# Kernel tuning notes

Measured on AMD Instinct MI355X. Metric: run time of the kernel, lower is better.

Reference implementation:

```python
import jax, jax.numpy as jnp
from jax import lax
import numpy as np

B, T, H = 128, 512, 512  # batch, seq_length, hidden_dim (== input_dim)


def _xavier(key, shape):
    fan_in, fan_out = shape[1], shape[0]
    limit = float(np.sqrt(6.0 / (fan_in + fan_out)))
    return jax.random.uniform(key, shape, jnp.float32, -limit, limit)


def setup_inputs() -> dict:
    key = jax.random.key(0)
    ks = jax.random.split(key, 10)
    s = 1.0 / np.sqrt(H)  # torch LSTM default init range
    return {
        "x": jax.random.normal(ks[0], (B, T, H), jnp.float32),
        "W_ih": jax.random.uniform(ks[1], (4 * H, H), jnp.float32, -s, s),
        "W_hh": jax.random.uniform(ks[2], (4 * H, H), jnp.float32, -s, s),
        "b_ih": jax.random.uniform(ks[3], (4 * H,), jnp.float32, -s, s),
        "b_hh": jax.random.uniform(ks[4], (4 * H,), jnp.float32, -s, s),
        "Ve": _xavier(ks[5], (1, H)),
        "U1": _xavier(ks[6], (H, 2 * H)),
        "U2": _xavier(ks[7], (H, H)),
        "W_out": _xavier(ks[8], (2, H)),
        "b_out": jnp.zeros((2,), jnp.float32),
    }


def _lstm(x, W_ih, W_hh, b_ih, b_hh):
    # x: [B, T, D] -> hidden states [B, T, H]; PyTorch gate order i,f,g,o
    b = b_ih + b_hh
    # precompute input projections for all timesteps: [T, B, 4H]
    xg = jnp.einsum('btd,gd->tbg', x, W_ih) + b

    def step(carry, xt):
        h, c = carry
        g = xt + h @ W_hh.T  # [B, 4H]
        i, f, gg, o = jnp.split(g, 4, axis=1)
        c = jax.nn.sigmoid(f) * c + jax.nn.sigmoid(i) * jnp.tanh(gg)
        h = jax.nn.sigmoid(o) * jnp.tanh(c)
        return (h, c), h

    h0 = jnp.zeros((x.shape[0], W_hh.shape[1]), x.dtype)
    (_, _), hs = lax.scan(step, (h0, h0), xg)
    return jnp.swapaxes(hs, 0, 1)  # [B, T, H]


def reference(x, W_ih, W_hh, b_ih, b_hh, Ve, U1, U2, W_out, b_out):
    h = _lstm(x, W_ih, W_hh, b_ih, b_hh)  # [B, T, H]
    h_last = h[:, -1, :]  # [B, H]
    # additive attention, vectorized over all timesteps
    Hdim = h.shape[-1]
    u1 = jnp.einsum('bth,gh->btg', h, U1[:, :Hdim]) + jnp.einsum('bh,gh->bg', h_last, U1[:, Hdim:])[:, None, :]
    u2 = jnp.einsum('btd,gd->btg', x, U2)
    u = jnp.tanh(u1 + u2)  # [B, T, H]
    e = jnp.einsum('bth,h->bt', u, Ve[0])
    alpha = jax.nn.softmax(e, axis=1)  # [B, T]
    context = jnp.einsum('bt,bth->bh', alpha, h)  # [B, H]
    params = context @ W_out.T + b_out  # [B, 2]
    mu = params[:, 0]
    sigma = jax.nn.softplus(params[:, 1]) + 1e-5
    return (mu, sigma)
```

## Files before the change

### kernel.cpp

```cpp
#include <hip/hip_runtime.h>
#include <stdint.h>


using short8  = __attribute__((ext_vector_type(8))) short;
using short4v = __attribute__((ext_vector_type(4))) short;
using floatx4 = __attribute__((ext_vector_type(4))) float;

#define MFMA16(a, b, c) __builtin_amdgcn_mfma_f32_16x16x32_bf16((a), (b), (c), 0, 0, 0)

__device__ __forceinline__ unsigned short f2b(float f) {
    unsigned u = __float_as_uint(f);
    u += 0x7FFFu + ((u >> 16) & 1u);
    return (unsigned short)(u >> 16);
}
__device__ __forceinline__ float b2f(unsigned short h) {
    return __uint_as_float(((unsigned)h) << 16);
}
__device__ __forceinline__ float sigm(float x) { return 1.0f / (1.0f + __expf(-x)); }
__device__ __forceinline__ float tanh_(float x) { return 1.0f - 2.0f / (__expf(2.0f * x) + 1.0f); }

__global__ __launch_bounds__(256) void prep_w(
    const float* __restrict__ Wih, const float* __restrict__ bih,
    const float* __restrict__ bhh,
    unsigned short* __restrict__ Wih_bf, float* __restrict__ bias)
{
    const int total = 1048576 + 2048;
    for (int i = blockIdx.x * 256 + threadIdx.x; i < total;
         i += gridDim.x * 256) {
        if (i < 1048576) Wih_bf[i] = f2b(Wih[i]);
        else             bias[i - 1048576] = bih[i - 1048576] + bhh[i - 1048576];
    }
}

__device__ __forceinline__ void gemm_core(
    const unsigned short* __restrict__ A, long long lda,
    const unsigned short* __restrict__ Bm, long long ldb,
    unsigned short* __restrict__ C, long long ldc,
    const float* __restrict__ bias, int mode,
    int m0, int n0, int tid, unsigned short* sbuf)
{
    unsigned short* At = sbuf;
    unsigned short* Bt = sbuf + 128 * 72;
    unsigned short* Ct = sbuf;

    const int wv = tid >> 6, lane = tid & 63, l15 = lane & 15, q = lane >> 4;
    const int wm = wv & 1, wn = wv >> 1;

    floatx4 acc[4][4];
    for (int i = 0; i < 4; i++)
        for (int j = 0; j < 4; j++) acc[i][j] = (floatx4){0.f, 0.f, 0.f, 0.f};

    for (int k0 = 0; k0 < 512; k0 += 64) {
        for (int p = 0; p < 4; p++) {
            int idx = tid + p * 256;
            int row = idx >> 3, ch = idx & 7;
            *(short8*)&At[row * 72 + ch * 8] =
                *(const short8*)&A[(long long)(m0 + row) * lda + k0 + ch * 8];
            *(short8*)&Bt[row * 72 + ch * 8] =
                *(const short8*)&Bm[(long long)(n0 + row) * ldb + k0 + ch * 8];
        }
        __syncthreads();
        for (int ks = 0; ks < 64; ks += 32) {
            short8 af[4], bfv[4];
            for (int mi = 0; mi < 4; mi++)
                af[mi] = *(const short8*)&At[(wm * 64 + mi * 16 + l15) * 72 + ks + q * 8];
            for (int ni = 0; ni < 4; ni++)
                bfv[ni] = *(const short8*)&Bt[(wn * 64 + ni * 16 + l15) * 72 + ks + q * 8];
            for (int mi = 0; mi < 4; mi++)
                for (int ni = 0; ni < 4; ni++)
                    acc[mi][ni] = MFMA16(af[mi], bfv[ni], acc[mi][ni]);
        }
        __syncthreads();
    }

    float bv[4];
    for (int ni = 0; ni < 4; ni++)
        bv[ni] = bias ? bias[n0 + wn * 64 + ni * 16 + l15] : 0.0f;

    for (int mi = 0; mi < 4; mi++)
        for (int ni = 0; ni < 4; ni++)
            for (int r = 0; r < 4; r++)
                Ct[(wm * 64 + mi * 16 + q * 4 + r) * 128 + wn * 64 + ni * 16 + l15] =
                    f2b(acc[mi][ni][r] + bv[ni]);
    __syncthreads();

    const int tt0 = m0 & 511, bglob = m0 >> 9;
    for (int p = 0; p < 8; p++) {
        int idx = tid + p * 256;
        int row = idx >> 4, ch = idx & 15;
        if (mode) {
            int n = n0 + ch * 8;
            int gate = n >> 9, jg = (n >> 4) & 31, c0 = gate * 16 + (n & 15);
            long long dst = (((long long)(tt0 + row) * 32 + jg) * 128 + bglob) * 64 + c0;
            *(short8*)&C[dst] = *(const short8*)&Ct[row * 128 + ch * 8];
        } else {
            *(short8*)&C[(long long)(m0 + row) * ldc + n0 + ch * 8] =
                *(const short8*)&Ct[row * 128 + ch * 8];
        }
    }
}

__device__ __forceinline__ void gemm_core_xf32(
    const float* __restrict__ Af, long long lda,
    const unsigned short* __restrict__ Bm,
    unsigned short* __restrict__ C,
    const float* __restrict__ bias,
    int m0, int n0, int tid, unsigned short* sbuf)
{
    unsigned short* At = sbuf;
    unsigned short* Bt = sbuf + 128 * 72;
    unsigned short* Ct = sbuf;

    const int wv = tid >> 6, lane = tid & 63, l15 = lane & 15, q = lane >> 4;
    const int wm = wv & 1, wn = wv >> 1;

    floatx4 acc[4][4];
    for (int i = 0; i < 4; i++)
        for (int j = 0; j < 4; j++) acc[i][j] = (floatx4){0.f, 0.f, 0.f, 0.f};

    for (int k0 = 0; k0 < 512; k0 += 64) {
        for (int p = 0; p < 4; p++) {
            int idx = tid + p * 256;
            int row = idx >> 3, ch = idx & 7;
            const float* ap = &Af[(long long)(m0 + row) * lda + k0 + ch * 8];
            float4 v0 = *(const float4*)ap;
            float4 v1 = *(const float4*)(ap + 4);
            short8 o;
            o[0] = (short)f2b(v0.x); o[1] = (short)f2b(v0.y);
            o[2] = (short)f2b(v0.z); o[3] = (short)f2b(v0.w);
            o[4] = (short)f2b(v1.x); o[5] = (short)f2b(v1.y);
            o[6] = (short)f2b(v1.z); o[7] = (short)f2b(v1.w);
            *(short8*)&At[row * 72 + ch * 8] = o;
            *(short8*)&Bt[row * 72 + ch * 8] =
                *(const short8*)&Bm[(long long)(n0 + row) * 512 + k0 + ch * 8];
        }
        __syncthreads();
        for (int ks = 0; ks < 64; ks += 32) {
            short8 af[4], bfv[4];
            for (int mi = 0; mi < 4; mi++)
                af[mi] = *(const short8*)&At[(wm * 64 + mi * 16 + l15) * 72 + ks + q * 8];
            for (int ni = 0; ni < 4; ni++)
                bfv[ni] = *(const short8*)&Bt[(wn * 64 + ni * 16 + l15) * 72 + ks + q * 8];
            for (int mi = 0; mi < 4; mi++)
                for (int ni = 0; ni < 4; ni++)
                    acc[mi][ni] = MFMA16(af[mi], bfv[ni], acc[mi][ni]);
        }
        __syncthreads();
    }

    float bv[4];
    for (int ni = 0; ni < 4; ni++)
        bv[ni] = bias[n0 + wn * 64 + ni * 16 + l15];

    for (int mi = 0; mi < 4; mi++)
        for (int ni = 0; ni < 4; ni++)
            for (int r = 0; r < 4; r++)
                Ct[(wm * 64 + mi * 16 + q * 4 + r) * 128 + wn * 64 + ni * 16 + l15] =
                    f2b(acc[mi][ni][r] + bv[ni]);
    __syncthreads();

    const int tt0 = m0 & 511, bglob = m0 >> 9;
    for (int p = 0; p < 8; p++) {
        int idx = tid + p * 256;
        int row = idx >> 4, ch = idx & 15;
        int n = n0 + ch * 8;
        int gate = n >> 9, jg = (n >> 4) & 31, c0 = gate * 16 + (n & 15);
        long long dst = (((long long)(tt0 + row) * 32 + jg) * 128 + bglob) * 64 + c0;
        *(short8*)&C[dst] = *(const short8*)&Ct[row * 128 + ch * 8];
    }
}

#define CONV_WGS 512
__global__ __launch_bounds__(256) void gemm_fused(
    const float* __restrict__ x, const float* __restrict__ Whh,
    const float* __restrict__ U1, const float* __restrict__ U2,
    unsigned short* __restrict__ x_bf, unsigned short* __restrict__ Whh_bf,
    unsigned short* __restrict__ U1a, unsigned short* __restrict__ U1b,
    unsigned short* __restrict__ U2b,
    const unsigned short* __restrict__ Wih_bf, const float* __restrict__ bias,
    unsigned short* __restrict__ xg_out)
{
    __shared__ __align__(16) unsigned short sbuf[2 * 128 * 72];
    const int tid = threadIdx.x;

    if (blockIdx.x < CONV_WGS) {
        const long long NX4 = 33554432LL / 4;
        const long long NREST = 1048576LL + 524288LL + 262144LL;
        const long long total = NX4 + NREST;
        for (long long u = (long long)blockIdx.x * 256 + tid; u < total;
             u += (long long)CONV_WGS * 256) {
            if (u < NX4) {
                float4 v = ((const float4*)x)[u];
                short4v o;
                o[0] = (short)f2b(v.x); o[1] = (short)f2b(v.y);
                o[2] = (short)f2b(v.z); o[3] = (short)f2b(v.w);
                *(short4v*)&x_bf[u * 4] = o;
            } else {
                long long i = u - NX4;
                if (i < 1048576) { Whh_bf[i] = f2b(Whh[i]); continue; }
                i -= 1048576;
                if (i < 524288) {
                    int row = (int)(i >> 10), col = (int)(i & 1023);
                    if (col < 512) U1a[row * 512 + col] = f2b(U1[i]);
                    else           U1b[row * 512 + (col - 512)] = f2b(U1[i]);
                    continue;
                }
                i -= 524288;
                U2b[i] = f2b(U2[i]);
            }
        }
        return;
    }

    const int g = blockIdx.x - CONV_WGS;
    const int b = g & 127, n = g >> 7;
    gemm_core_xf32(x, 512, Wih_bf, xg_out, bias, b * 512, n * 128, tid, sbuf);
}

template<int NNI>
__device__ __forceinline__ void attn_helper_body(
    const unsigned short* __restrict__ h_all,
    const unsigned short* __restrict__ x_bf,
    const unsigned short* __restrict__ U1a,
    const unsigned short* __restrict__ U2b,
    unsigned short* __restrict__ xg_out,
    int* __restrict__ syncp,
    int b, int t0, int nBase, int tid, char* smem)
{
    const int bg = b >> 4;
    if (tid < 8) {
        while (__hip_atomic_load(&syncp[16 + (bg * 8 + tid) * 16],
                                 __ATOMIC_RELAXED,
                                 __HIP_MEMORY_SCOPE_AGENT) < t0 + 32)
            __builtin_amdgcn_s_sleep(8);
    }
    __syncthreads();

    unsigned short* Bt2 = (unsigned short*)smem;
    unsigned short* At2 = (unsigned short*)smem + (NNI * 64) * 40;

    const int wv = tid >> 6, lane = tid & 63, l15 = lane & 15, q = lane >> 4;

    floatx4 acc[2][NNI];
    #pragma unroll
    for (int mi = 0; mi < 2; mi++)
        #pragma unroll
        for (int ni = 0; ni < NNI; ni++) acc[mi][ni] = (floatx4){0.f, 0.f, 0.f, 0.f};

    for (int it = 0; it < 32; it++) {
        const int phase = it >> 4, kk = (it & 15) * 32;
        const unsigned short* Bsrc = phase ? U2b : U1a;
        __syncthreads();
        #pragma unroll
        for (int pp = 0; pp < NNI; pp++) {
            int idx = tid + pp * 256;
            int row = idx >> 2, ch = idx & 3;
            *(short8*)&Bt2[row * 40 + ch * 8] =
                *(const short8*)&Bsrc[(long long)(nBase + row) * 512 + kk + ch * 8];
        }
        if (tid < 128) {
            int row = tid >> 2, ch = tid & 3;
            if (phase == 0) {
                unsigned long long* p = (unsigned long long*)
                    &h_all[((long long)b * 512 + t0 + row) * 512 + kk + ch * 8];
                unsigned long long lo = __hip_atomic_load(p, __ATOMIC_RELAXED,
                                                          __HIP_MEMORY_SCOPE_AGENT);
                unsigned long long hi = __hip_atomic_load(p + 1, __ATOMIC_RELAXED,
                                                          __HIP_MEMORY_SCOPE_AGENT);
                unsigned long long* d = (unsigned long long*)&At2[row * 40 + ch * 8];
                d[0] = lo; d[1] = hi;
            } else {
                *(short8*)&At2[row * 40 + ch * 8] =
                    *(const short8*)&x_bf[((long long)b * 512 + t0 + row) * 512 + kk + ch * 8];
            }
        }
        __syncthreads();
        short8 af0 = *(const short8*)&At2[(l15) * 40 + q * 8];
        short8 af1 = *(const short8*)&At2[(16 + l15) * 40 + q * 8];
        #pragma unroll
        for (int ni = 0; ni < NNI; ni++) {
            short8 bfv = *(const short8*)&Bt2[(wv * (NNI * 16) + ni * 16 + l15) * 40 + q * 8];
            acc[0][ni] = MFMA16(af0, bfv, acc[0][ni]);
            acc[1][ni] = MFMA16(af1, bfv, acc[1][ni]);
        }
    }
    #pragma unroll
    for (int mi = 0; mi < 2; mi++)
        #pragma unroll
        for (int ni = 0; ni < NNI; ni++) {
            const int n = nBase + wv * (NNI * 16) + ni * 16 + l15;
            #pragma unroll
            for (int r = 0; r < 4; r++) {
                const int t = t0 + mi * 16 + q * 4 + r;
                float* slot = (float*)&xg_out[(((long long)t * 32 + (n >> 5)) * 128 + b) * 64];
                slot[n & 31] = acc[mi][ni][r];
            }
        }
}

#define GEMM_WGS 6144
#define ATTN_WGS 2432
__global__ __launch_bounds__(256, 1) void mega(
    const unsigned short* __restrict__ xg,
    const unsigned short* __restrict__ Whh,
    unsigned short* __restrict__ h_all,
    unsigned int* __restrict__ ring,
    const unsigned short* __restrict__ x_bf,
    const unsigned short* __restrict__ Wih_bf,
    const float* __restrict__ bias,
    unsigned short* __restrict__ xg_out,
    int* __restrict__ syncp,
    const unsigned short* __restrict__ U1a,
    const unsigned short* __restrict__ U2b)
{
    __shared__ __align__(16) char smem[86016];

    const int tid = threadIdx.x;

    if (blockIdx.x >= 64 && blockIdx.x < 64 + GEMM_WGS) {
        int g = blockIdx.x - 64;
        int b = g & 127;
        int r = g >> 7;
        int ti = 1 + (r % 3);
        int n = r / 3;
        gemm_core(x_bf, 512, Wih_bf, 512, xg_out, 2048, bias, 1,
                  b * 512 + ti * 128, n * 128, tid, (unsigned short*)smem);
        __syncthreads();
        if (tid == 0)
            __hip_atomic_fetch_add(&syncp[0], 1, __ATOMIC_RELEASE,
                                   __HIP_MEMORY_SCOPE_AGENT);
        return;
    }

    if (blockIdx.x >= 64 + GEMM_WGS) {
        const int g = blockIdx.x - 64 - GEMM_WGS;
        if (g < 1920) {
            attn_helper_body<8>(h_all, x_bf, U1a, U2b, xg_out, syncp,
                                g & 127, (g >> 7) * 32, 0, tid, smem);
        } else {
            const int j = g - 1920;
            attn_helper_body<2>(h_all, x_bf, U1a, U2b, xg_out, syncp,
                                j & 127, 480, (j >> 7) * 128, tid, smem);
        }
        return;
    }

    unsigned int (*At)[16 * 264] = (unsigned int (*)[16 * 264])smem;

    const int wv = tid >> 6, lane = tid & 63, l15 = lane & 15, q = lane >> 4;
    const int bg = blockIdx.x >> 3, jgb = blockIdx.x & 7;
    const int b0 = bg * 16;
    const int jg32 = jgb * 4 + wv;
    const int hid = jg32 * 16 + l15;

    short8 Wreg[4][16];
    #pragma unroll
    for (int ct = 0; ct < 4; ct++)
        #pragma unroll
        for (int kk = 0; kk < 16; kk++)
            Wreg[ct][kk] = *(const short8*)
                &Whh[(long long)(ct * 512 + hid) * 512 + kk * 32 + q * 8];

    float cst[4] = {0.f, 0.f, 0.f, 0.f};

    for (int t = 0; t < 512; t++) {
        if (t == 128) {
            if (tid == 0) {
                while (__hip_atomic_load(&syncp[0], __ATOMIC_ACQUIRE,
                                         __HIP_MEMORY_SCOPE_AGENT) < GEMM_WGS)
                    __builtin_amdgcn_s_sleep(8);
            }
            __syncthreads();
        }
        const long long xbase = ((long long)(t * 32 + jg32) * 128 + b0) * 64;
        floatx4 acc[4];
        #pragma unroll
        for (int ct = 0; ct < 4; ct++)
            #pragma unroll
            for (int r = 0; r < 4; r++)
                acc[ct][r] = b2f(xg[xbase + (q * 4 + r) * 64 + ct * 16 + l15]);

        if (t > 0) {
            const unsigned want = (unsigned)(t - 1);
            const int sl = (t - 1) & 1;
            unsigned long long* rb = (unsigned long long*)
                (ring + sl * 65536 + b0 * 512);
            unsigned long long w[16];
            #pragma unroll
            for (int i = 0; i < 16; i++)
                w[i] = __hip_atomic_load(&rb[tid + i * 256], __ATOMIC_RELAXED,
                                         __HIP_MEMORY_SCOPE_AGENT);
            while (true) {
                unsigned bad = 0;
                #pragma unroll
                for (int i = 0; i < 16; i++) {
                    unsigned lo = (unsigned)(w[i] >> 16) & 0xFFFFu;
                    unsigned hi = (unsigned)(w[i] >> 48);
                    bad |= (lo ^ want) | (hi ^ want);
                }
                if (!bad) break;
                #pragma unroll
                for (int i = 0; i < 16; i++) {
                    unsigned lo = (unsigned)(w[i] >> 16) & 0xFFFFu;
                    unsigned hi = (unsigned)(w[i] >> 48);
                    if ((lo ^ want) | (hi ^ want))
                        w[i] = __hip_atomic_load(&rb[tid + i * 256], __ATOMIC_RELAXED,
                                                 __HIP_MEMORY_SCOPE_AGENT);
                }
            }
            unsigned int* dst = &At[sl][0];
            #pragma unroll
            for (int i = 0; i < 16; i++) {
                int idx = tid + i * 256;
                int row = idx >> 8, k = idx & 255;
                dst[row * 264 + k] =
                    (unsigned)(w[i] & 0xFFFFu) | ((unsigned)(w[i] >> 32) << 16);
            }
            __syncthreads();
            const unsigned int* ap = &At[sl][l15 * 264 + q * 4];
            #pragma unroll
            for (int kk = 0; kk < 16; kk++) {
                short8 af = *(const short8*)(ap + kk * 16);
                acc[0] = MFMA16(af, Wreg[0][kk], acc[0]);
                acc[1] = MFMA16(af, Wreg[1][kk], acc[1]);
                acc[2] = MFMA16(af, Wreg[2][kk], acc[2]);
                acc[3] = MFMA16(af, Wreg[3][kk], acc[3]);
            }
        }
        unsigned short hbv[4];
        #pragma unroll
        for (int r = 0; r < 4; r++) {
            float ig = sigm(acc[0][r]);
            float fg = sigm(acc[1][r]);
            float gv = tanh_(acc[2][r]);
            float og = sigm(acc[3][r]);
            cst[r] = fg * cst[r] + ig * gv;
            hbv[r] = f2b(og * tanh_(cst[r]));
        }
        #pragma unroll
        for (int r = 0; r < 4; r++) {
            const int b = b0 + q * 4 + r;
            __hip_atomic_store(&ring[(t & 1) * 65536 + b * 512 + hid],
                               ((unsigned)t << 16) | hbv[r], __ATOMIC_RELAXED,
                               __HIP_MEMORY_SCOPE_AGENT);
        }
        #pragma unroll
        for (int r = 0; r < 4; r++) {
            const int b = b0 + q * 4 + r;
            int o = __shfl_xor((int)hbv[r], 1);
            if (!(l15 & 1)) {
                unsigned v = (unsigned)hbv[r] | (((unsigned)(unsigned short)o) << 16);
                __hip_atomic_store(
                    (unsigned*)&h_all[(long long)b * 262144 + (long long)t * 512 + hid],
                    v, __ATOMIC_RELAXED, __HIP_MEMORY_SCOPE_AGENT);
            }
        }
        if ((t & 15) == 15) {
            __syncthreads();
            if (tid == 0)
                __hip_atomic_store(&syncp[16 + (int)blockIdx.x * 16], t + 1,
                                   __ATOMIC_RELAXED, __HIP_MEMORY_SCOPE_AGENT);
        }
    }
}

__global__ __launch_bounds__(256) void attn_out(
    const unsigned short* __restrict__ a_xg,
    const unsigned short* __restrict__ h_all,
    const unsigned short* __restrict__ U1b,
    const float* __restrict__ Ve,
    const float* __restrict__ Wout, const float* __restrict__ bout,
    float* __restrict__ outp)
{
    __shared__ float hl[512];
    __shared__ float u1s[512];
    __shared__ float se[512];
    __shared__ float sm[512];
    __shared__ float red[8];
    const int b = blockIdx.x, tid = threadIdx.x;
    const int wv = tid >> 6, lane = tid & 63;

    {
        unsigned v = ((const unsigned*)(h_all + (long long)b * 262144 + 511LL * 512))[tid];
        hl[2 * tid]     = b2f((unsigned short)(v & 0xFFFFu));
        hl[2 * tid + 1] = b2f((unsigned short)(v >> 16));
    }
    __syncthreads();
    #pragma unroll
    for (int rr = 0; rr < 2; rr++) {
        const int n = tid + rr * 256;
        const unsigned short* up = &U1b[(long long)n * 512];
        float s = 0.f;
        for (int k = 0; k < 512; k += 8) {
            short8 v8 = *(const short8*)&up[k];
            #pragma unroll
            for (int j = 0; j < 8; j++)
                s += hl[k + j] * b2f((unsigned short)v8[j]);
        }
        u1s[n] = s;
    }
    __syncthreads();

    const int n0 = lane * 8;
    float ve[8], ub[8];
    #pragma unroll
    for (int j = 0; j < 8; j++) {
        ve[j] = Ve[n0 + j];
        ub[j] = u1s[n0 + j];
    }
    for (int it = 0; it < 64; it++) {
        const int t = it * 8 + wv * 2;
        const float* s0p = (const float*)
            &a_xg[(((long long)t * 32 + (n0 >> 5)) * 128 + b) * 64];
        const float* s1p = (const float*)
            &a_xg[(((long long)(t + 1) * 32 + (n0 >> 5)) * 128 + b) * 64];
        float4 a0 = *(const float4*)&s0p[n0 & 31];
        float4 a1 = *(const float4*)&s0p[(n0 & 31) + 4];
        float4 a2 = *(const float4*)&s1p[n0 & 31];
        float4 a3 = *(const float4*)&s1p[(n0 & 31) + 4];
        float s0 = ve[0] * tanh_(a0.x + ub[0]) + ve[1] * tanh_(a0.y + ub[1])
                 + ve[2] * tanh_(a0.z + ub[2]) + ve[3] * tanh_(a0.w + ub[3])
                 + ve[4] * tanh_(a1.x + ub[4]) + ve[5] * tanh_(a1.y + ub[5])
                 + ve[6] * tanh_(a1.z + ub[6]) + ve[7] * tanh_(a1.w + ub[7]);
        float s1 = ve[0] * tanh_(a2.x + ub[0]) + ve[1] * tanh_(a2.y + ub[1])
                 + ve[2] * tanh_(a2.z + ub[2]) + ve[3] * tanh_(a2.w + ub[3])
                 + ve[4] * tanh_(a3.x + ub[4]) + ve[5] * tanh_(a3.y + ub[5])
                 + ve[6] * tanh_(a3.z + ub[6]) + ve[7] * tanh_(a3.w + ub[7]);
        #pragma unroll
        for (int off = 1; off <= 32; off <<= 1) {
            s0 += __shfl_xor(s0, off);
            s1 += __shfl_xor(s1, off);
        }
        if (lane == 0) { se[t] = s0; se[t + 1] = s1; }
    }
    __syncthreads();

    float e0 = se[tid], e1 = se[256 + tid];
    float mx = fmaxf(e0, e1);
    for (int off = 32; off; off >>= 1) mx = fmaxf(mx, __shfl_xor(mx, off));
    if (lane == 0) red[wv] = mx;
    __syncthreads();
    mx = fmaxf(fmaxf(red[0], red[1]), fmaxf(red[2], red[3]));

    float s0 = __expf(e0 - mx), s1 = __expf(e1 - mx);
    sm[tid] = s0; sm[256 + tid] = s1;
    float ss = s0 + s1;
    for (int off = 32; off; off >>= 1) ss += __shfl_xor(ss, off);
    if (lane == 0) red[4 + wv] = ss;
    __syncthreads();
    float inv = 1.0f / (red[4] + red[5] + red[6] + red[7]);

    const unsigned int* hp = (const unsigned int*)(h_all + (long long)b * 262144);
    float a0 = 0.f, a1 = 0.f;
    for (int t = 0; t < 512; t += 4) {
        #pragma unroll
        for (int j = 0; j < 4; j++) {
            float al = sm[t + j];
            unsigned v = hp[(t + j) * 256 + tid];
            a0 += al * b2f((unsigned short)(v & 0xFFFFu));
            a1 += al * b2f((unsigned short)(v >> 16));
        }
    }
    a0 *= inv; a1 *= inv;

    float q0 = a0 * Wout[2 * tid] + a1 * Wout[2 * tid + 1];
    float q1 = a0 * Wout[512 + 2 * tid] + a1 * Wout[512 + 2 * tid + 1];
    for (int off = 32; off; off >>= 1) { q0 += __shfl_xor(q0, off); q1 += __shfl_xor(q1, off); }
    __syncthreads();
    if (lane == 0) { red[wv] = q0; red[4 + wv] = q1; }
    __syncthreads();
    if (tid == 0) {
        float P0 = red[0] + red[1] + red[2] + red[3] + bout[0];
        float P1 = red[4] + red[5] + red[6] + red[7] + bout[1];
        outp[b] = P0;
        float sp = (P1 > 15.0f) ? P1 : log1pf(__expf(P1));
        outp[128 + b] = sp + 1e-5f;
    }
}

extern "C" void kernel_launch(void* const* d_in, const int* in_sizes, int n_in,
                              void* d_out, int out_size, void* d_ws, size_t ws_size,
                              hipStream_t stream)
{
    const float* x    = (const float*)d_in[0];
    const float* Wih  = (const float*)d_in[1];
    const float* Whh  = (const float*)d_in[2];
    const float* bih  = (const float*)d_in[3];
    const float* bhh  = (const float*)d_in[4];
    const float* Ve   = (const float*)d_in[5];
    const float* U1   = (const float*)d_in[6];
    const float* U2   = (const float*)d_in[7];
    const float* Wout = (const float*)d_in[8];
    const float* bout = (const float*)d_in[9];
    float* out = (float*)d_out;

    char* ws = (char*)d_ws;
    size_t off = 0;
    auto alloc = [&](size_t bytes) -> void* {
        void* p = ws + off;
        off += (bytes + 255) & ~(size_t)255;
        return p;
    };
    unsigned short* x_bf   = (unsigned short*)alloc(33554432ull * 2);
    unsigned short* Wih_bf = (unsigned short*)alloc(1048576ull * 2);
    unsigned short* Whh_bf = (unsigned short*)alloc(1048576ull * 2);
    unsigned short* U1a    = (unsigned short*)alloc(262144ull * 2);
    unsigned short* U1b    = (unsigned short*)alloc(262144ull * 2);
    unsigned short* U2b    = (unsigned short*)alloc(262144ull * 2);
    float*          bias   = (float*)alloc(2048ull * 4);
    unsigned short* xg     = (unsigned short*)alloc(134217728ull * 2);
    unsigned short* h_all  = (unsigned short*)alloc(33554432ull * 2);
    unsigned int*   ring   = (unsigned int*)alloc(131072ull * 4);
    int*            syncp  = (int*)alloc(8192ull);
    if (off > ws_size) return;

    hipMemsetAsync(syncp, 0, 8192, stream);
    prep_w<<<1024, 256, 0, stream>>>(Wih, bih, bhh, Wih_bf, bias);
    gemm_fused<<<CONV_WGS + 2048, 256, 0, stream>>>(
        x, Whh, U1, U2, x_bf, Whh_bf, U1a, U1b, U2b, Wih_bf, bias, xg);
    mega<<<64 + GEMM_WGS + ATTN_WGS, 256, 0, stream>>>(
        xg, Whh_bf, h_all, ring, x_bf, Wih_bf, bias, xg, syncp, U1a, U2b);
    attn_out<<<128, 256, 0, stream>>>(xg, h_all, U1b, Ve, Wout, bout, out);
}
```

Before: 2.592 ms.

## Fold weight prep and first input-projection GEMM into persistent mega kernel

```diff
diff --git a/kernel.cpp b/kernel.cpp
--- a/kernel.cpp
+++ b/kernel.cpp
@@ -19,24 +19,27 @@
 __device__ __forceinline__ float sigm(float x) { return 1.0f / (1.0f + __expf(-x)); }
 __device__ __forceinline__ float tanh_(float x) { return 1.0f - 2.0f / (__expf(2.0f * x) + 1.0f); }
 
-__global__ __launch_bounds__(256) void prep_w(
-    const float* __restrict__ Wih, const float* __restrict__ bih,
-    const float* __restrict__ bhh,
-    unsigned short* __restrict__ Wih_bf, float* __restrict__ bias)
-{
-    const int total = 1048576 + 2048;
-    for (int i = blockIdx.x * 256 + threadIdx.x; i < total;
-         i += gridDim.x * 256) {
-        if (i < 1048576) Wih_bf[i] = f2b(Wih[i]);
-        else             bias[i - 1048576] = bih[i - 1048576] + bhh[i - 1048576];
-    }
-}
-
-__device__ __forceinline__ void gemm_core(
+__device__ __forceinline__ short8 cvt8(const float* __restrict__ p) {
+    float4 v0 = *(const float4*)p;
+    float4 v1 = *(const float4*)(p + 4);
+    short8 o;
+    o[0] = (short)f2b(v0.x); o[1] = (short)f2b(v0.y);
+    o[2] = (short)f2b(v0.z); o[3] = (short)f2b(v0.w);
+    o[4] = (short)f2b(v1.x); o[5] = (short)f2b(v1.y);
+    o[6] = (short)f2b(v1.z); o[7] = (short)f2b(v1.w);
+    return o;
+}
+
+#define TI0_WGS   2048
+#define CONV_WGS  512
+#define TI123_WGS 6144
+#define ATTN_WGS  2432
+
+__device__ __forceinline__ void gemm_core_bf(
     const unsigned short* __restrict__ A, long long lda,
-    const unsigned short* __restrict__ Bm, long long ldb,
-    unsigned short* __restrict__ C, long long ldc,
-    const float* __restrict__ bias, int mode,
+    const unsigned short* __restrict__ Bm,
+    unsigned short* __restrict__ C,
+    const float* __restrict__ bih, const float* __restrict__ bhh,
     int m0, int n0, int tid, unsigned short* sbuf)
 {
     unsigned short* At = sbuf;
@@ -57,7 +60,7 @@
             *(short8*)&At[row * 72 + ch * 8] =
                 *(const short8*)&A[(long long)(m0 + row) * lda + k0 + ch * 8];
             *(short8*)&Bt[row * 72 + ch * 8] =
-                *(const short8*)&Bm[(long long)(n0 + row) * ldb + k0 + ch * 8];
+                *(const short8*)&Bm[(long long)(n0 + row) * 512 + k0 + ch * 8];
         }
         __syncthreads();
         for (int ks = 0; ks < 64; ks += 32) {
@@ -74,8 +77,10 @@
     }
 
     float bv[4];
-    for (int ni = 0; ni < 4; ni++)
-        bv[ni] = bias ? bias[n0 + wn * 64 + ni * 16 + l15] : 0.0f;
+    for (int ni = 0; ni < 4; ni++) {
+        int nn = n0 + wn * 64 + ni * 16 + l15;
+        bv[ni] = bih[nn] + bhh[nn];
+    }
 
     for (int mi = 0; mi < 4; mi++)
         for (int ni = 0; ni < 4; ni++)
@@ -88,24 +93,19 @@
     for (int p = 0; p < 8; p++) {
         int idx = tid + p * 256;
         int row = idx >> 4, ch = idx & 15;
-        if (mode) {
-            int n = n0 + ch * 8;
-            int gate = n >> 9, jg = (n >> 4) & 31, c0 = gate * 16 + (n & 15);
-            long long dst = (((long long)(tt0 + row) * 32 + jg) * 128 + bglob) * 64 + c0;
-            *(short8*)&C[dst] = *(const short8*)&Ct[row * 128 + ch * 8];
-        } else {
-            *(short8*)&C[(long long)(m0 + row) * ldc + n0 + ch * 8] =
-                *(const short8*)&Ct[row * 128 + ch * 8];
-        }
-    }
-}
-
-__device__ __forceinline__ void gemm_core_xf32(
-    const float* __restrict__ Af, long long lda,
-    const unsigned short* __restrict__ Bm,
+        int n = n0 + ch * 8;
+        int gate = n >> 9, jg = (n >> 4) & 31, c0 = gate * 16 + (n & 15);
+        long long dst = (((long long)(tt0 + row) * 32 + jg) * 128 + bglob) * 64 + c0;
+        *(short8*)&C[dst] = *(const short8*)&Ct[row * 128 + ch * 8];
+    }
+}
+
+__device__ __forceinline__ void gemm_core_ti0(
+    const float* __restrict__ x,
+    const float* __restrict__ Wih,
     unsigned short* __restrict__ C,
-    const float* __restrict__ bias,
-    int m0, int n0, int tid, unsigned short* sbuf)
+    const float* __restrict__ bih, const float* __restrict__ bhh,
+    int b0, int t0, int n0, int tid, unsigned short* sbuf)
 {
     unsigned short* At = sbuf;
     unsigned short* Bt = sbuf + 128 * 72;
@@ -122,17 +122,11 @@
         for (int p = 0; p < 4; p++) {
             int idx = tid + p * 256;
             int row = idx >> 3, ch = idx & 7;
-            const float* ap = &Af[(long long)(m0 + row) * lda + k0 + ch * 8];
-            float4 v0 = *(const float4*)ap;
-            float4 v1 = *(const float4*)(ap + 4);
-            short8 o;
-            o[0] = (short)f2b(v0.x); o[1] = (short)f2b(v0.y);
-            o[2] = (short)f2b(v0.z); o[3] = (short)f2b(v0.w);
-            o[4] = (short)f2b(v1.x); o[5] = (short)f2b(v1.y);
-            o[6] = (short)f2b(v1.z); o[7] = (short)f2b(v1.w);
-            *(short8*)&At[row * 72 + ch * 8] = o;
+            int bq = row >> 5, tq = row & 31;
+            *(short8*)&At[row * 72 + ch * 8] =
+                cvt8(&x[((long long)(b0 + bq) * 512 + t0 + tq) * 512 + k0 + ch * 8]);
             *(short8*)&Bt[row * 72 + ch * 8] =
-                *(const short8*)&Bm[(long long)(n0 + row) * 512 + k0 + ch * 8];
+                cvt8(&Wih[(long long)(n0 + row) * 512 + k0 + ch * 8]);
         }
         __syncthreads();
         for (int ks = 0; ks < 64; ks += 32) {
@@ -149,8 +143,10 @@
     }
 
     float bv[4];
-    for (int ni = 0; ni < 4; ni++)
-        bv[ni] = bias[n0 + wn * 64 + ni * 16 + l15];
+    for (int ni = 0; ni < 4; ni++) {
+        int nn = n0 + wn * 64 + ni * 16 + l15;
+        bv[ni] = bih[nn] + bhh[nn];
+    }
 
     for (int mi = 0; mi < 4; mi++)
         for (int ni = 0; ni < 4; ni++)
@@ -159,62 +155,15 @@
                     f2b(acc[mi][ni][r] + bv[ni]);
     __syncthreads();
 
-    const int tt0 = m0 & 511, bglob = m0 >> 9;
     for (int p = 0; p < 8; p++) {
         int idx = tid + p * 256;
         int row = idx >> 4, ch = idx & 15;
+        int bq = row >> 5, tq = row & 31;
         int n = n0 + ch * 8;
         int gate = n >> 9, jg = (n >> 4) & 31, c0 = gate * 16 + (n & 15);
-        long long dst = (((long long)(tt0 + row) * 32 + jg) * 128 + bglob) * 64 + c0;
+        long long dst = (((long long)(t0 + tq) * 32 + jg) * 128 + (b0 + bq)) * 64 + c0;
         *(short8*)&C[dst] = *(const short8*)&Ct[row * 128 + ch * 8];
     }
-}
-
-#define CONV_WGS 512
-__global__ __launch_bounds__(256) void gemm_fused(
-    const float* __restrict__ x, const float* __restrict__ Whh,
-    const float* __restrict__ U1, const float* __restrict__ U2,
-    unsigned short* __restrict__ x_bf, unsigned short* __restrict__ Whh_bf,
-    unsigned short* __restrict__ U1a, unsigned short* __restrict__ U1b,
-    unsigned short* __restrict__ U2b,
-    const unsigned short* __restrict__ Wih_bf, const float* __restrict__ bias,
-    unsigned short* __restrict__ xg_out)
-{
-    __shared__ __align__(16) unsigned short sbuf[2 * 128 * 72];
-    const int tid = threadIdx.x;
-
-    if (blockIdx.x < CONV_WGS) {
-        const long long NX4 = 33554432LL / 4;
-        const long long NREST = 1048576LL + 524288LL + 262144LL;
-        const long long total = NX4 + NREST;
-        for (long long u = (long long)blockIdx.x * 256 + tid; u < total;
-             u += (long long)CONV_WGS * 256) {
-            if (u < NX4) {
-                float4 v = ((const float4*)x)[u];
-                short4v o;
-                o[0] = (short)f2b(v.x); o[1] = (short)f2b(v.y);
-                o[2] = (short)f2b(v.z); o[3] = (short)f2b(v.w);
-                *(short4v*)&x_bf[u * 4] = o;
-            } else {
-                long long i = u - NX4;
-                if (i < 1048576) { Whh_bf[i] = f2b(Whh[i]); continue; }
-                i -= 1048576;
-                if (i < 524288) {
-                    int row = (int)(i >> 10), col = (int)(i & 1023);
-                    if (col < 512) U1a[row * 512 + col] = f2b(U1[i]);
-                    else           U1b[row * 512 + (col - 512)] = f2b(U1[i]);
-                    continue;
-                }
-                i -= 524288;
-                U2b[i] = f2b(U2[i]);
-            }
-        }
-        return;
-    }
-
-    const int g = blockIdx.x - CONV_WGS;
-    const int b = g & 127, n = g >> 7;
-    gemm_core_xf32(x, 512, Wih_bf, xg_out, bias, b * 512, n * 128, tid, sbuf);
 }
 
 template<int NNI>
@@ -233,6 +182,10 @@
                                  __ATOMIC_RELAXED,
                                  __HIP_MEMORY_SCOPE_AGENT) < t0 + 32)
             __builtin_amdgcn_s_sleep(8);
+    } else if (tid == 8) {
+        while (__hip_atomic_load(&syncp[8], __ATOMIC_ACQUIRE,
+                                 __HIP_MEMORY_SCOPE_AGENT) < CONV_WGS)
+            __builtin_amdgcn_s_sleep(8);
     }
     __syncthreads();
 
@@ -298,33 +251,90 @@
         }
 }
 
-#define GEMM_WGS 6144
-#define ATTN_WGS 2432
 __global__ __launch_bounds__(256, 1) void mega(
-    const unsigned short* __restrict__ xg,
-    const unsigned short* __restrict__ Whh,
+    const float* __restrict__ x,
+    const float* __restrict__ Wih,
+    const float* __restrict__ Whh,
+    const float* __restrict__ bih, const float* __restrict__ bhh,
+    const float* __restrict__ U1, const float* __restrict__ U2,
+    unsigned short* __restrict__ x_bf,
+    unsigned short* __restrict__ Wih_bf,
+    unsigned short* __restrict__ U1a, unsigned short* __restrict__ U1b,
+    unsigned short* __restrict__ U2b,
+    unsigned short* __restrict__ xg,
     unsigned short* __restrict__ h_all,
     unsigned int* __restrict__ ring,
-    const unsigned short* __restrict__ x_bf,
-    const unsigned short* __restrict__ Wih_bf,
-    const float* __restrict__ bias,
-    unsigned short* __restrict__ xg_out,
-    int* __restrict__ syncp,
-    const unsigned short* __restrict__ U1a,
-    const unsigned short* __restrict__ U2b)
+    int* __restrict__ syncp)
 {
     __shared__ __align__(16) char smem[86016];
 
     const int tid = threadIdx.x;
-
-    if (blockIdx.x >= 64 && blockIdx.x < 64 + GEMM_WGS) {
-        int g = blockIdx.x - 64;
+    const int bid = (int)blockIdx.x;
+
+    if (bid >= 64 && bid < 64 + TI0_WGS) {
+        int g = bid - 64;
+        int tb = g >> 9;
+        int r = g & 511;
+        int b0 = (r & 31) * 4;
+        int n0 = (r >> 5) * 128;
+        gemm_core_ti0(x, Wih, xg, bih, bhh, b0, tb * 32, n0, tid,
+                      (unsigned short*)smem);
+        __syncthreads();
+        if (tid == 0)
+            __hip_atomic_fetch_add(&syncp[1 + tb], 1, __ATOMIC_RELEASE,
+                                   __HIP_MEMORY_SCOPE_AGENT);
+        return;
+    }
+
+    if (bid >= 64 + TI0_WGS && bid < 64 + TI0_WGS + CONV_WGS) {
+        const long long NX4 = 33554432LL / 4;
+        const long long NREST = 1048576LL + 524288LL + 262144LL;
+        const long long total = NX4 + NREST;
+        const int cb = bid - (64 + TI0_WGS);
+        for (long long u = (long long)cb * 256 + tid; u < total;
+             u += (long long)CONV_WGS * 256) {
+            if (u < NX4) {
+                float4 v = ((const float4*)x)[u];
+                short4v o;
+                o[0] = (short)f2b(v.x); o[1] = (short)f2b(v.y);
+                o[2] = (short)f2b(v.z); o[3] = (short)f2b(v.w);
+                *(short4v*)&x_bf[u * 4] = o;
+            } else {
+                long long i = u - NX4;
+                if (i < 1048576) { Wih_bf[i] = f2b(Wih[i]); continue; }
+                i -= 1048576;
+                if (i < 524288) {
+                    int row = (int)(i >> 10), col = (int)(i & 1023);
+                    if (col < 512) U1a[row * 512 + col] = f2b(U1[i]);
+                    else           U1b[row * 512 + (col - 512)] = f2b(U1[i]);
+                    continue;
+                }
+                i -= 524288;
+                U2b[i] = f2b(U2[i]);
+            }
+        }
+        __syncthreads();
+        if (tid == 0)
+            __hip_atomic_fetch_add(&syncp[8], 1, __ATOMIC_RELEASE,
+                                   __HIP_MEMORY_SCOPE_AGENT);
+        return;
+    }
+
+    if (bid >= 64 + TI0_WGS + CONV_WGS &&
+        bid < 64 + TI0_WGS + CONV_WGS + TI123_WGS) {
+        if (tid == 0) {
+            while (__hip_atomic_load(&syncp[8], __ATOMIC_ACQUIRE,
+                                     __HIP_MEMORY_SCOPE_AGENT) < CONV_WGS)
+                __builtin_amdgcn_s_sleep(8);
+        }
+        __syncthreads();
+        int g = bid - (64 + TI0_WGS + CONV_WGS);
         int b = g & 127;
         int r = g >> 7;
         int ti = 1 + (r % 3);
         int n = r / 3;
-        gemm_core(x_bf, 512, Wih_bf, 512, xg_out, 2048, bias, 1,
-                  b * 512 + ti * 128, n * 128, tid, (unsigned short*)smem);
+        gemm_core_bf(x_bf, 512, Wih_bf, xg, bih, bhh,
+                     b * 512 + ti * 128, n * 128, tid, (unsigned short*)smem);
         __syncthreads();
         if (tid == 0)
             __hip_atomic_fetch_add(&syncp[0], 1, __ATOMIC_RELEASE,
@@ -332,14 +342,14 @@
         return;
     }
 
-    if (blockIdx.x >= 64 + GEMM_WGS) {
-        const int g = blockIdx.x - 64 - GEMM_WGS;
+    if (bid >= 64 + TI0_WGS + CONV_WGS + TI123_WGS) {
+        const int g = bid - (64 + TI0_WGS + CONV_WGS + TI123_WGS);
         if (g < 1920) {
-            attn_helper_body<8>(h_all, x_bf, U1a, U2b, xg_out, syncp,
+            attn_helper_body<8>(h_all, x_bf, U1a, U2b, xg, syncp,
                                 g & 127, (g >> 7) * 32, 0, tid, smem);
         } else {
             const int j = g - 1920;
-            attn_helper_body<2>(h_all, x_bf, U1a, U2b, xg_out, syncp,
+            attn_helper_body<2>(h_all, x_bf, U1a, U2b, xg, syncp,
                                 j & 127, 480, (j >> 7) * 128, tid, smem);
         }
         return;
@@ -348,7 +358,7 @@
     unsigned int (*At)[16 * 264] = (unsigned int (*)[16 * 264])smem;
 
     const int wv = tid >> 6, lane = tid & 63, l15 = lane & 15, q = lane >> 4;
-    const int bg = blockIdx.x >> 3, jgb = blockIdx.x & 7;
+    const int bg = bid >> 3, jgb = bid & 7;
     const int b0 = bg * 16;
     const int jg32 = jgb * 4 + wv;
     const int hid = jg32 * 16 + l15;
@@ -358,17 +368,22 @@
     for (int ct = 0; ct < 4; ct++)
         #pragma unroll
         for (int kk = 0; kk < 16; kk++)
-            Wreg[ct][kk] = *(const short8*)
-                &Whh[(long long)(ct * 512 + hid) * 512 + kk * 32 + q * 8];
+            Wreg[ct][kk] = cvt8(&Whh[(long long)(ct * 512 + hid) * 512 + kk * 32 + q * 8]);
 
     float cst[4] = {0.f, 0.f, 0.f, 0.f};
 
     for (int t = 0; t < 512; t++) {
-        if (t == 128) {
+        if ((t & 31) == 0 && t <= 128) {
             if (tid == 0) {
-                while (__hip_atomic_load(&syncp[0], __ATOMIC_ACQUIRE,
-                                         __HIP_MEMORY_SCOPE_AGENT) < GEMM_WGS)
-                    __builtin_amdgcn_s_sleep(8);
+                if (t < 128) {
+                    while (__hip_atomic_load(&syncp[1 + (t >> 5)], __ATOMIC_ACQUIRE,
+                                             __HIP_MEMORY_SCOPE_AGENT) < 512)
+                        __builtin_amdgcn_s_sleep(8);
+                } else {
+                    while (__hip_atomic_load(&syncp[0], __ATOMIC_ACQUIRE,
+                                             __HIP_MEMORY_SCOPE_AGENT) < TI123_WGS)
+                        __builtin_amdgcn_s_sleep(8);
+                }
             }
             __syncthreads();
         }
@@ -458,7 +473,7 @@
         if ((t & 15) == 15) {
             __syncthreads();
             if (tid == 0)
-                __hip_atomic_store(&syncp[16 + (int)blockIdx.x * 16], t + 1,
+                __hip_atomic_store(&syncp[16 + bid * 16], t + 1,
                                    __ATOMIC_RELAXED, __HIP_MEMORY_SCOPE_AGENT);
         }
     }
@@ -603,11 +618,9 @@
     };
     unsigned short* x_bf   = (unsigned short*)alloc(33554432ull * 2);
     unsigned short* Wih_bf = (unsigned short*)alloc(1048576ull * 2);
-    unsigned short* Whh_bf = (unsigned short*)alloc(1048576ull * 2);
     unsigned short* U1a    = (unsigned short*)alloc(262144ull * 2);
     unsigned short* U1b    = (unsigned short*)alloc(262144ull * 2);
     unsigned short* U2b    = (unsigned short*)alloc(262144ull * 2);
-    float*          bias   = (float*)alloc(2048ull * 4);
     unsigned short* xg     = (unsigned short*)alloc(134217728ull * 2);
     unsigned short* h_all  = (unsigned short*)alloc(33554432ull * 2);
     unsigned int*   ring   = (unsigned int*)alloc(131072ull * 4);
@@ -615,10 +628,8 @@
     if (off > ws_size) return;
 
     hipMemsetAsync(syncp, 0, 8192, stream);
-    prep_w<<<1024, 256, 0, stream>>>(Wih, bih, bhh, Wih_bf, bias);
-    gemm_fused<<<CONV_WGS + 2048, 256, 0, stream>>>(
-        x, Whh, U1, U2, x_bf, Whh_bf, U1a, U1b, U2b, Wih_bf, bias, xg);
-    mega<<<64 + GEMM_WGS + ATTN_WGS, 256, 0, stream>>>(
-        xg, Whh_bf, h_all, ring, x_bf, Wih_bf, bias, xg, syncp, U1a, U2b);
+    mega<<<64 + TI0_WGS + CONV_WGS + TI123_WGS + ATTN_WGS, 256, 0, stream>>>(
+        x, Wih, Whh, bih, bhh, U1, U2,
+        x_bf, Wih_bf, U1a, U1b, U2b, xg, h_all, ring, syncp);
     attn_out<<<128, 256, 0, stream>>>(xg, h_all, U1b, Ve, Wout, bout, out);
 }
```

Result: slower. 2.997 ms (+15.6%).
